# Kernel optimization log

Measured on AMD Instinct MI355X. Metric: run time of the kernel, lower is better.

Reference implementation:

```python
import jax, jax.numpy as jnp
import numpy as np


def setup_inputs() -> dict:
    key = jax.random.key(0)
    B, D = 256, 4096
    continuous_input = jax.random.normal(key, (B, D), dtype=jnp.float32)
    return {"continuous_input": continuous_input, "timesteps": 100}


def reference(continuous_input, timesteps):
    # Temporal coding: each (batch, input) pair fires exactly one spike at a
    # time determined by sigmoid(value). With num_neurons == input_dim the
    # neuron index is just the input index, so the scalar scatter in the
    # original nested Python loops is exactly a one-hot over the time axis.
    T = timesteps
    # torch .long() truncates; sigmoid*(T-1) >= 0 so floor == trunc
    spike_times = jnp.floor(jax.nn.sigmoid(continuous_input) * (T - 1)).astype(jnp.int32)  # [B, D]
    t = jnp.arange(T, dtype=jnp.int32)  # [T]
    spikes = (t[:, None, None] == spike_times[None, :, :]).astype(jnp.float32)  # [T, B, N]
    return spikes
```

## Files before the change

kernel.cpp:

```cpp
#include <hip/hip_runtime.h>
#include <math.h>


typedef __attribute__((ext_vector_type(4))) float f32x4;

__device__ __forceinline__ float sigmoidf(float x) {
    return 1.0f / (1.0f + expf(-x));
}

__global__ __launch_bounds__(256) void temporal_encoder_kernel(
    const float* __restrict__ x, float* __restrict__ out,
    int n , int T) {
    const int tid = blockIdx.x * blockDim.x + threadIdx.x;
    const int e = tid * 4;
    if (e + 3 < n) {
        f32x4 v = *reinterpret_cast<const f32x4*>(x + e);
        const float tm1 = (float)(T - 1);
        const int st0 = (int)(sigmoidf(v.x) * tm1);
        const int st1 = (int)(sigmoidf(v.y) * tm1);
        const int st2 = (int)(sigmoidf(v.z) * tm1);
        const int st3 = (int)(sigmoidf(v.w) * tm1);
        float* p = out + e;
        for (int t = 0; t < T; ++t) {
            f32x4 o;
            o.x = (t == st0) ? 1.0f : 0.0f;
            o.y = (t == st1) ? 1.0f : 0.0f;
            o.z = (t == st2) ? 1.0f : 0.0f;
            o.w = (t == st3) ? 1.0f : 0.0f;
            *reinterpret_cast<f32x4*>(p) = o;
            p += n;
        }
    } else if (e < n) {
        const float tm1 = (float)(T - 1);
        for (int i = e; i < n; ++i) {
            const int st = (int)(sigmoidf(x[i]) * tm1);
            float* p = out + i;
            for (int t = 0; t < T; ++t) {
                *p = (t == st) ? 1.0f : 0.0f;
                p += n;
            }
        }
    }
}

extern "C" void kernel_launch(void* const* d_in, const int* in_sizes, int n_in,
                              void* d_out, int out_size, void* d_ws, size_t ws_size,
                              hipStream_t stream) {
    const float* x = (const float*)d_in[0];
    float* out = (float*)d_out;
    const int n = in_sizes[0];
    const int T = out_size / n;
    const int threads = 256;
    const int vec_elems = 4;
    const int nthreads_total = (n + vec_elems - 1) / vec_elems;
    const int blocks = (nthreads_total + threads - 1) / threads;
    temporal_encoder_kernel<<<blocks, threads, 0, stream>>>(x, out, n, T);
}
```

Baseline: 426.0 us.

## Precompute spike times and parallelize one-hot writes over a 2D grid

Splits the encoder into a kernel that computes spike times into a byte workspace and a second kernel launched over a (blocks, T) grid where each thread writes one float4 per timestep. This replaces the per-thread serial loop over T with many independent threads, aiming to raise store parallelism. A fused fallback recomputes the sigmoid per timestep when no workspace is available. It adds an extra launch and restricts spike times to fit in a byte.

```diff
diff --git a/kernel.cpp b/kernel.cpp
--- a/kernel.cpp
+++ b/kernel.cpp
@@ -8,38 +8,57 @@
     return 1.0f / (1.0f + expf(-x));
 }
 
-__global__ __launch_bounds__(256) void temporal_encoder_kernel(
-    const float* __restrict__ x, float* __restrict__ out,
-    int n , int T) {
-    const int tid = blockIdx.x * blockDim.x + threadIdx.x;
-    const int e = tid * 4;
+__global__ __launch_bounds__(256) void spike_time_kernel(
+    const float* __restrict__ x, unsigned char* __restrict__ st,
+    int n, float tm1) {
+    const int e = (blockIdx.x * 256 + threadIdx.x) * 4;
     if (e + 3 < n) {
         f32x4 v = *reinterpret_cast<const f32x4*>(x + e);
-        const float tm1 = (float)(T - 1);
-        const int st0 = (int)(sigmoidf(v.x) * tm1);
-        const int st1 = (int)(sigmoidf(v.y) * tm1);
-        const int st2 = (int)(sigmoidf(v.z) * tm1);
-        const int st3 = (int)(sigmoidf(v.w) * tm1);
-        float* p = out + e;
-        for (int t = 0; t < T; ++t) {
-            f32x4 o;
-            o.x = (t == st0) ? 1.0f : 0.0f;
-            o.y = (t == st1) ? 1.0f : 0.0f;
-            o.z = (t == st2) ? 1.0f : 0.0f;
-            o.w = (t == st3) ? 1.0f : 0.0f;
-            *reinterpret_cast<f32x4*>(p) = o;
-            p += n;
-        }
-    } else if (e < n) {
-        const float tm1 = (float)(T - 1);
-        for (int i = e; i < n; ++i) {
-            const int st = (int)(sigmoidf(x[i]) * tm1);
-            float* p = out + i;
-            for (int t = 0; t < T; ++t) {
-                *p = (t == st) ? 1.0f : 0.0f;
-                p += n;
-            }
-        }
+        uchar4 s;
+        s.x = (unsigned char)(int)(sigmoidf(v.x) * tm1);
+        s.y = (unsigned char)(int)(sigmoidf(v.y) * tm1);
+        s.z = (unsigned char)(int)(sigmoidf(v.z) * tm1);
+        s.w = (unsigned char)(int)(sigmoidf(v.w) * tm1);
+        *reinterpret_cast<uchar4*>(st + e) = s;
+    } else {
+        for (int i = e; i < n; ++i)
+            st[i] = (unsigned char)(int)(sigmoidf(x[i]) * tm1);
+    }
+}
+
+__global__ __launch_bounds__(256) void write_onehot_kernel(
+    const unsigned char* __restrict__ st, float* __restrict__ out, int n) {
+    const int t = blockIdx.y;
+    const int e = (blockIdx.x * 256 + threadIdx.x) * 4;
+    if (e + 3 < n) {
+        uchar4 s = *reinterpret_cast<const uchar4*>(st + e);
+        f32x4 o;
+        o.x = (s.x == t) ? 1.0f : 0.0f;
+        o.y = (s.y == t) ? 1.0f : 0.0f;
+        o.z = (s.z == t) ? 1.0f : 0.0f;
+        o.w = (s.w == t) ? 1.0f : 0.0f;
+        *reinterpret_cast<f32x4*>(out + (size_t)t * n + e) = o;
+    } else {
+        for (int i = e; i < n; ++i)
+            out[(size_t)t * n + i] = (st[i] == t) ? 1.0f : 0.0f;
+    }
+}
+
+__global__ __launch_bounds__(256) void fused_onehot_kernel(
+    const float* __restrict__ x, float* __restrict__ out, int n, float tm1) {
+    const int t = blockIdx.y;
+    const int e = (blockIdx.x * 256 + threadIdx.x) * 4;
+    if (e + 3 < n) {
+        f32x4 v = *reinterpret_cast<const f32x4*>(x + e);
+        f32x4 o;
+        o.x = ((int)(sigmoidf(v.x) * tm1) == t) ? 1.0f : 0.0f;
+        o.y = ((int)(sigmoidf(v.y) * tm1) == t) ? 1.0f : 0.0f;
+        o.z = ((int)(sigmoidf(v.z) * tm1) == t) ? 1.0f : 0.0f;
+        o.w = ((int)(sigmoidf(v.w) * tm1) == t) ? 1.0f : 0.0f;
+        *reinterpret_cast<f32x4*>(out + (size_t)t * n + e) = o;
+    } else {
+        for (int i = e; i < n; ++i)
+            out[(size_t)t * n + i] = ((int)(sigmoidf(x[i]) * tm1) == t) ? 1.0f : 0.0f;
     }
 }
 
@@ -50,9 +69,18 @@
     float* out = (float*)d_out;
     const int n = in_sizes[0];
     const int T = out_size / n;
-    const int threads = 256;
-    const int vec_elems = 4;
-    const int nthreads_total = (n + vec_elems - 1) / vec_elems;
-    const int blocks = (nthreads_total + threads - 1) / threads;
-    temporal_encoder_kernel<<<blocks, threads, 0, stream>>>(x, out, n, T);
+    const float tm1 = (float)(T - 1);
+
+    const int n4 = (n + 3) / 4;
+    const int blocks_x = (n4 + 255) / 256;
+
+    if (ws_size >= (size_t)n) {
+        unsigned char* st = (unsigned char*)d_ws;
+        spike_time_kernel<<<blocks_x, 256, 0, stream>>>(x, st, n, tm1);
+        dim3 grid(blocks_x, T);
+        write_onehot_kernel<<<grid, 256, 0, stream>>>(st, out, n);
+    } else {
+        dim3 grid(blocks_x, T);
+        fused_onehot_kernel<<<grid, 256, 0, stream>>>(x, out, n, tm1);
+    }
 }
```

Measured after the change: 401.6 us. 5.7% less time.
